# Kernel optimization log

Measured on AMD Instinct MI355X. Metric: run time of the kernel, lower is better.

## Reference

```python
import jax, jax.numpy as jnp
import numpy as np
from jax import lax

NUM_INPUTS = 1024
NUM_OUTPUTS = 1024
NUM_LAYERS = 32          # 1 first + (NUM_LAYERS-1) middle + 1 last, per torch __init__
N = 4096                 # num_neurons_per_layer
W = 65536                # parallel bit-array width


def _nand_layer(x, idx, mask):
    # x: [num_in, W] bool; idx: [num_out, 2] int; mask: [num_out] bool
    g = x[idx]                       # [num_out, 2, W] gather
    out = g[:, 0, :] & g[:, 1, :]    # bitwise AND
    return jnp.where(mask[:, None], ~out, out)  # conditional NOT


def setup_inputs() -> dict:
    key = jax.random.key(0)
    k = jax.random.split(key, 7)
    n_mid = NUM_LAYERS - 1
    return {
        "input_bitarrays": jax.random.bernoulli(k[0], 0.5, (NUM_INPUTS, W)),
        "idx_first": jax.random.randint(k[1], (N, 2), 0, NUM_INPUTS, dtype=jnp.int64 if jax.config.jax_enable_x64 else jnp.int32),
        "mask_first": jax.random.bernoulli(k[2], 0.5, (N,)),
        "idx_mid": jax.random.randint(k[3], (n_mid, N, 2), 0, N, dtype=jnp.int64 if jax.config.jax_enable_x64 else jnp.int32),
        "mask_mid": jax.random.bernoulli(k[4], 0.5, (n_mid, N)),
        "idx_last": jax.random.randint(k[5], (NUM_OUTPUTS, 2), 0, N, dtype=jnp.int64 if jax.config.jax_enable_x64 else jnp.int32),
        "mask_last": jax.random.bernoulli(k[6], 0.5, (NUM_OUTPUTS,)),
    }


def reference(input_bitarrays, idx_first, mask_first, idx_mid, mask_mid, idx_last, mask_last):
    x = _nand_layer(input_bitarrays, idx_first, mask_first)

    def step(carry, params):
        idx, mask = params
        return _nand_layer(carry, idx, mask), None

    x, _ = lax.scan(step, x, (idx_mid, mask_mid))
    return _nand_layer(x, idx_last, mask_last)
```

## Files before the change

### kernel.cpp

```cpp
#include <hip/hip_runtime.h>
#include <stdint.h>

#define NINPUTS   1024
#define NOUTPUTS  1024
#define NMID      31
#define NN        4096
#define W         65536
#define CHUNK     128
#define WPN       4
#define NCHUNKS   (W / CHUNK)
#define GRID      256
#define CPW       (NCHUNKS / GRID)
#define THREADS   1024
#define NPAIRS    16
#define TBL_BYTES ((size_t)NPAIRS * NN * 16)

__global__ void build_tbl_kernel(const int*      __restrict__ idx_first,
                                 const uint32_t* __restrict__ mask_first,
                                 const int*      __restrict__ idx_mid,
                                 const uint32_t* __restrict__ mask_mid,
                                 uint4*          __restrict__ tbl)
{
    const int tid = blockIdx.x * blockDim.x + threadIdx.x;
    const int F = tid >> 12;
    const int n = tid & (NN - 1);

    const int*      i1;
    const uint32_t* m1;
    if (F == 0) { i1 = idx_first; m1 = mask_first; }
    else        { i1 = idx_mid + (size_t)(2 * F - 1) * NN * 2;
                  m1 = mask_mid + (size_t)(2 * F - 1) * NN; }
    const int*      i2 = idx_mid + (size_t)(2 * F) * NN * 2;
    const uint32_t* m2 = mask_mid + (size_t)(2 * F) * NN;

    const int j = i2[2 * n];
    const int k = i2[2 * n + 1];
    uint4 e;
    e.x = (uint32_t)(i1[2 * j]     * 16) | (m1[j] ? 0x80000000u : 0u);
    e.y = (uint32_t)(i1[2 * j + 1] * 16);
    e.z = (uint32_t)(i1[2 * k]     * 16) | (m1[k] ? 0x80000000u : 0u);
    e.w = (uint32_t)(i1[2 * k + 1] * 16) | (m2[n] ? 0x80000000u : 0u);
    tbl[(size_t)F * NN + n] = e;
}

__global__ __launch_bounds__(THREADS, 4)
void nand_fused_kernel(const uint32_t* __restrict__ in,
                       const uint4*    __restrict__ tbl,
                       const int*      __restrict__ idx_last,
                       const uint32_t* __restrict__ mask_last,
                       uint32_t*       __restrict__ out)
{
    __shared__ uint32_t lds[40960];
    uint32_t* P = lds;
    uint32_t* X = lds + 4096;
    uint32_t* Y = lds + 20480;
    uint32_t* R = lds + 36864;

    const int t      = threadIdx.x;
    const int l      = t & 63;
    const int wv     = t >> 6;
    const int lane32 = l & 31;
    const int half   = l >> 5;
    const int shift  = half ? 32 : 0;
    const int bcol   = blockIdx.x * (CPW * CHUNK);

    #pragma unroll 4
    for (int s = 0; s < 32; ++s) {
        const int r = s * 32 + wv * 2 + half;
        const uint4 v = *(const uint4*)(in + (size_t)r * W + bcol + lane32 * 4);
        const unsigned long long b0 = __ballot(v.x != 0u);
        const unsigned long long b1 = __ballot(v.y != 0u);
        const unsigned long long b2 = __ballot(v.z != 0u);
        const unsigned long long b3 = __ballot(v.w != 0u);
        if (lane32 == 0) {
            uint4 w;
            w.x = (uint32_t)(b0 >> shift);
            w.y = (uint32_t)(b1 >> shift);
            w.z = (uint32_t)(b2 >> shift);
            w.w = (uint32_t)(b3 >> shift);
            *(uint4*)&P[r * WPN] = w;
        }
    }
    __syncthreads();

    for (int i = 0; i < CPW; ++i) {
        const int c0n = bcol + (i + 1) * CHUNK;
        const int c0p = bcol + (i - 1) * CHUNK;
        const bool do_pack   = (i + 1 < CPW);
        const bool do_unpack = (i > 0);

        uint4 tc[4], tn[4];
        #pragma unroll
        for (int k = 0; k < 4; ++k) tc[k] = tbl[k * THREADS + t];

        for (int F = 0; F <= 16; ++F) {
            uint4 pv0 = {0,0,0,0}, pv1 = {0,0,0,0};
            int pr0 = 0, pr1 = 0;
            if (do_pack && F >= 1) {
                pr0 = (F - 1) * 64 + wv * 2 + half;
                pr1 = pr0 + 32;
                pv0 = *(const uint4*)(in + (size_t)pr0 * W + c0n + lane32 * 4);
                pv1 = *(const uint4*)(in + (size_t)pr1 * W + c0n + lane32 * 4);
            }

            if (F <= 15) {
                const uint32_t* src = (F == 0) ? P : ((F & 1) ? X : Y);
                uint32_t*       dst = (F & 1) ? Y : X;
                uint4 A[4], B[4], C[4], D[4];
                #pragma unroll
                for (int k = 0; k < 4; ++k) {
                    const uint4 e = tc[k];
                    A[k] = *(const uint4*)((const char*)src + (e.x & 0xFFFFu));
                    B[k] = *(const uint4*)((const char*)src + e.y);
                    C[k] = *(const uint4*)((const char*)src + (e.z & 0xFFFFu));
                    D[k] = *(const uint4*)((const char*)src + (e.w & 0xFFFFu));
                }
                #pragma unroll
                for (int k = 0; k < 4; ++k) {
                    const int n = k * THREADS + t;
                    const uint4 e = tc[k];
                    const uint32_t xm1 = (uint32_t)((int32_t)e.x >> 31);
                    const uint32_t xm2 = (uint32_t)((int32_t)e.z >> 31);
                    const uint32_t xm3 = (uint32_t)((int32_t)e.w >> 31);
                    uint4 r;
                    r.x = (((A[k].x & B[k].x) ^ xm1) & ((C[k].x & D[k].x) ^ xm2)) ^ xm3;
                    r.y = (((A[k].y & B[k].y) ^ xm1) & ((C[k].y & D[k].y) ^ xm2)) ^ xm3;
                    r.z = (((A[k].z & B[k].z) ^ xm1) & ((C[k].z & D[k].z) ^ xm2)) ^ xm3;
                    r.w = (((A[k].w & B[k].w) ^ xm1) & ((C[k].w & D[k].w) ^ xm2)) ^ xm3;
                    *(uint4*)&dst[n * WPN] = r;
                }
            } else {
                const int n = t;
                const int2 ij = ((const int2*)idx_last)[n];
                const uint32_t xm = mask_last[n] ? 0xFFFFFFFFu : 0u;
                const uint4 a = *(const uint4*)&Y[ij.x * WPN];
                const uint4 b = *(const uint4*)&Y[ij.y * WPN];
                uint4 r;
                r.x = (a.x & b.x) ^ xm;  r.y = (a.y & b.y) ^ xm;
                r.z = (a.z & b.z) ^ xm;  r.w = (a.w & b.w) ^ xm;
                *(uint4*)&R[n * WPN] = r;
            }

            if (F <= 14) {
                #pragma unroll
                for (int k = 0; k < 4; ++k)
                    tn[k] = tbl[(size_t)(F + 1) * NN + k * THREADS + t];
            }

            if (do_unpack && F <= 15) {
                #pragma unroll
                for (int s = 0; s < 2; ++s) {
                    const int r = F * 64 + s * 32 + wv * 2 + half;
                    const uint4 w4 = *(const uint4*)&R[r * WPN];
                    uint4 v;
                    v.x = (w4.x >> lane32) & 1u;
                    v.y = (w4.y >> lane32) & 1u;
                    v.z = (w4.z >> lane32) & 1u;
                    v.w = (w4.w >> lane32) & 1u;
                    *(uint4*)(out + (size_t)r * W + c0p + lane32 * 4) = v;
                }
            }

            if (do_pack && F >= 1) {
                {
                    const unsigned long long b0 = __ballot(pv0.x != 0u);
                    const unsigned long long b1 = __ballot(pv0.y != 0u);
                    const unsigned long long b2 = __ballot(pv0.z != 0u);
                    const unsigned long long b3 = __ballot(pv0.w != 0u);
                    if (lane32 == 0) {
                        uint4 w;
                        w.x = (uint32_t)(b0 >> shift);
                        w.y = (uint32_t)(b1 >> shift);
                        w.z = (uint32_t)(b2 >> shift);
                        w.w = (uint32_t)(b3 >> shift);
                        *(uint4*)&P[pr0 * WPN] = w;
                    }
                }
                {
                    const unsigned long long b0 = __ballot(pv1.x != 0u);
                    const unsigned long long b1 = __ballot(pv1.y != 0u);
                    const unsigned long long b2 = __ballot(pv1.z != 0u);
                    const unsigned long long b3 = __ballot(pv1.w != 0u);
                    if (lane32 == 0) {
                        uint4 w;
                        w.x = (uint32_t)(b0 >> shift);
                        w.y = (uint32_t)(b1 >> shift);
                        w.z = (uint32_t)(b2 >> shift);
                        w.w = (uint32_t)(b3 >> shift);
                        *(uint4*)&P[pr1 * WPN] = w;
                    }
                }
            }

            if (F <= 14) {
                #pragma unroll
                for (int k = 0; k < 4; ++k) tc[k] = tn[k];
            }
            __syncthreads();
        }
    }

    {
        const int c0l = bcol + (CPW - 1) * CHUNK;
        #pragma unroll 4
        for (int s = 0; s < 32; ++s) {
            const int r = s * 32 + wv * 2 + half;
            const uint4 w4 = *(const uint4*)&R[r * WPN];
            uint4 v;
            v.x = (w4.x >> lane32) & 1u;
            v.y = (w4.y >> lane32) & 1u;
            v.z = (w4.z >> lane32) & 1u;
            v.w = (w4.w >> lane32) & 1u;
            *(uint4*)(out + (size_t)r * W + c0l + lane32 * 4) = v;
        }
    }
}

__global__ __launch_bounds__(THREADS, 4)
void nand_pipe128_kernel(const uint32_t* __restrict__ in,
                         const int*      __restrict__ idx_first,
                         const uint32_t* __restrict__ mask_first,
                         const int*      __restrict__ idx_mid,
                         const uint32_t* __restrict__ mask_mid,
                         const int*      __restrict__ idx_last,
                         const uint32_t* __restrict__ mask_last,
                         uint32_t*       __restrict__ out)
{
    __shared__ uint32_t lds[40960];
    uint32_t* P = lds;
    uint32_t* X = lds + 4096;
    uint32_t* Y = lds + 20480;
    uint32_t* R = lds + 36864;

    const int t      = threadIdx.x;
    const int l      = t & 63;
    const int wv     = t >> 6;
    const int lane32 = l & 31;
    const int half   = l >> 5;
    const int shift  = half ? 32 : 0;
    const int bcol   = blockIdx.x * (CPW * CHUNK);

    #pragma unroll 4
    for (int s = 0; s < 32; ++s) {
        const int r = s * 32 + wv * 2 + half;
        const uint4 v = *(const uint4*)(in + (size_t)r * W + bcol + lane32 * 4);
        const unsigned long long b0 = __ballot(v.x != 0u);
        const unsigned long long b1 = __ballot(v.y != 0u);
        const unsigned long long b2 = __ballot(v.z != 0u);
        const unsigned long long b3 = __ballot(v.w != 0u);
        if (lane32 == 0) {
            uint4 w;
            w.x = (uint32_t)(b0 >> shift);  w.y = (uint32_t)(b1 >> shift);
            w.z = (uint32_t)(b2 >> shift);  w.w = (uint32_t)(b3 >> shift);
            *(uint4*)&P[r * WPN] = w;
        }
    }
    __syncthreads();

    for (int i = 0; i < CPW; ++i) {
        const int c0n = bcol + (i + 1) * CHUNK;
        const int c0p = bcol + (i - 1) * CHUNK;
        const bool do_pack   = (i + 1 < CPW);
        const bool do_unpack = (i > 0);

        for (int L = 0; L <= 32; ++L) {
            uint4 pv = {0, 0, 0, 0};
            int   pr = 0;
            if (do_pack && L >= 1) {
                pr = (L - 1) * 32 + wv * 2 + half;
                pv = *(const uint4*)(in + (size_t)pr * W + c0n + lane32 * 4);
            }
            if (L == 0) {
                #pragma unroll
                for (int k = 0; k < NN / THREADS; ++k) {
                    const int n = k * THREADS + t;
                    const int2 ij = ((const int2*)idx_first)[n];
                    const uint32_t xm = mask_first[n] ? 0xFFFFFFFFu : 0u;
                    const uint4 a = *(const uint4*)&P[ij.x * WPN];
                    const uint4 b = *(const uint4*)&P[ij.y * WPN];
                    uint4 r;
                    r.x = (a.x & b.x) ^ xm;  r.y = (a.y & b.y) ^ xm;
                    r.z = (a.z & b.z) ^ xm;  r.w = (a.w & b.w) ^ xm;
                    *(uint4*)&X[n * WPN] = r;
                }
            } else if (L <= 31) {
                const int*      idxL = idx_mid + (size_t)(L - 1) * NN * 2;
                const uint32_t* mL   = mask_mid + (size_t)(L - 1) * NN;
                const uint32_t* src  = (L & 1) ? X : Y;
                uint32_t*       dst  = (L & 1) ? Y : X;
                #pragma unroll
                for (int k = 0; k < NN / THREADS; ++k) {
                    const int n = k * THREADS + t;
                    const int2 ij = ((const int2*)idxL)[n];
                    const uint32_t xm = mL[n] ? 0xFFFFFFFFu : 0u;
                    const uint4 a = *(const uint4*)&src[ij.x * WPN];
                    const uint4 b = *(const uint4*)&src[ij.y * WPN];
                    uint4 r;
                    r.x = (a.x & b.x) ^ xm;  r.y = (a.y & b.y) ^ xm;
                    r.z = (a.z & b.z) ^ xm;  r.w = (a.w & b.w) ^ xm;
                    *(uint4*)&dst[n * WPN] = r;
                }
            } else {
                const int n = t;
                const int2 ij = ((const int2*)idx_last)[n];
                const uint32_t xm = mask_last[n] ? 0xFFFFFFFFu : 0u;
                const uint4 a = *(const uint4*)&Y[ij.x * WPN];
                const uint4 b = *(const uint4*)&Y[ij.y * WPN];
                uint4 r;
                r.x = (a.x & b.x) ^ xm;  r.y = (a.y & b.y) ^ xm;
                r.z = (a.z & b.z) ^ xm;  r.w = (a.w & b.w) ^ xm;
                *(uint4*)&R[n * WPN] = r;
            }
            if (do_unpack && L <= 31) {
                const int r = L * 32 + wv * 2 + half;
                const uint4 w4 = *(const uint4*)&R[r * WPN];
                uint4 v;
                v.x = (w4.x >> lane32) & 1u;  v.y = (w4.y >> lane32) & 1u;
                v.z = (w4.z >> lane32) & 1u;  v.w = (w4.w >> lane32) & 1u;
                *(uint4*)(out + (size_t)r * W + c0p + lane32 * 4) = v;
            }
            if (do_pack && L >= 1) {
                const unsigned long long b0 = __ballot(pv.x != 0u);
                const unsigned long long b1 = __ballot(pv.y != 0u);
                const unsigned long long b2 = __ballot(pv.z != 0u);
                const unsigned long long b3 = __ballot(pv.w != 0u);
                if (lane32 == 0) {
                    uint4 w;
                    w.x = (uint32_t)(b0 >> shift);  w.y = (uint32_t)(b1 >> shift);
                    w.z = (uint32_t)(b2 >> shift);  w.w = (uint32_t)(b3 >> shift);
                    *(uint4*)&P[pr * WPN] = w;
                }
            }
            __syncthreads();
        }
    }
    {
        const int c0l = bcol + (CPW - 1) * CHUNK;
        #pragma unroll 4
        for (int s = 0; s < 32; ++s) {
            const int r = s * 32 + wv * 2 + half;
            const uint4 w4 = *(const uint4*)&R[r * WPN];
            uint4 v;
            v.x = (w4.x >> lane32) & 1u;  v.y = (w4.y >> lane32) & 1u;
            v.z = (w4.z >> lane32) & 1u;  v.w = (w4.w >> lane32) & 1u;
            *(uint4*)(out + (size_t)r * W + c0l + lane32 * 4) = v;
        }
    }
}

extern "C" void kernel_launch(void* const* d_in, const int* in_sizes, int n_in,
                              void* d_out, int out_size, void* d_ws, size_t ws_size,
                              hipStream_t stream) {
    const uint32_t* in         = (const uint32_t*)d_in[0];
    const int*      idx_first  = (const int*)d_in[1];
    const uint32_t* mask_first = (const uint32_t*)d_in[2];
    const int*      idx_mid    = (const int*)d_in[3];
    const uint32_t* mask_mid   = (const uint32_t*)d_in[4];
    const int*      idx_last   = (const int*)d_in[5];
    const uint32_t* mask_last  = (const uint32_t*)d_in[6];
    uint32_t*       out        = (uint32_t*)d_out;

    if (ws_size >= TBL_BYTES) {
        uint4* tbl = (uint4*)d_ws;
        build_tbl_kernel<<<(NPAIRS * NN) / 256, 256, 0, stream>>>(
            idx_first, mask_first, idx_mid, mask_mid, tbl);
        nand_fused_kernel<<<GRID, THREADS, 0, stream>>>(
            in, tbl, idx_last, mask_last, out);
    } else {
        nand_pipe128_kernel<<<GRID, THREADS, 0, stream>>>(
            in, idx_first, mask_first, idx_mid, mask_mid, idx_last, mask_last, out);
    }
}
```

Baseline: 151.9 us.

## Store intermediate LDS layers in struct-of-arrays layout with ds_read2st64 gathers

The X and Y intermediate buffers switch from an array-of-structs layout (four words per neuron) to a struct-of-arrays layout where each word plane is strided by 4096 words. Gathers and stores use ds_read2st64/ds_write2st64 inline asm, and the table offsets are rescaled to match. The goal is to cut LDS bank conflicts from random 16-byte gathers. In exchange, each k iteration now waits on lgkmcnt(0) behind a sched_barrier, which limits overlap of LDS loads across the unrolled k loop, and the prefetch of the next table is moved earlier.

```diff
diff --git a/kernel.cpp b/kernel.cpp
--- a/kernel.cpp
+++ b/kernel.cpp
@@ -15,6 +15,9 @@
 #define NPAIRS    16
 #define TBL_BYTES ((size_t)NPAIRS * NN * 16)
 
+#define XB 16384u
+#define YB 81920u
+
 __global__ void build_tbl_kernel(const int*      __restrict__ idx_first,
                                  const uint32_t* __restrict__ mask_first,
                                  const int*      __restrict__ idx_mid,
@@ -33,15 +36,28 @@
     const int*      i2 = idx_mid + (size_t)(2 * F) * NN * 2;
     const uint32_t* m2 = mask_mid + (size_t)(2 * F) * NN;
 
+    const uint32_t scale = (F == 0) ? 16u : 4u;
     const int j = i2[2 * n];
     const int k = i2[2 * n + 1];
     uint4 e;
-    e.x = (uint32_t)(i1[2 * j]     * 16) | (m1[j] ? 0x80000000u : 0u);
-    e.y = (uint32_t)(i1[2 * j + 1] * 16);
-    e.z = (uint32_t)(i1[2 * k]     * 16) | (m1[k] ? 0x80000000u : 0u);
-    e.w = (uint32_t)(i1[2 * k + 1] * 16) | (m2[n] ? 0x80000000u : 0u);
+    e.x = (uint32_t)i1[2 * j]     * scale | (m1[j] ? 0x80000000u : 0u);
+    e.y = (uint32_t)i1[2 * j + 1] * scale;
+    e.z = (uint32_t)i1[2 * k]     * scale | (m1[k] ? 0x80000000u : 0u);
+    e.w = (uint32_t)i1[2 * k + 1] * scale | (m2[n] ? 0x80000000u : 0u);
     tbl[(size_t)F * NN + n] = e;
 }
+
+#define SOA_READ(W01, W23, VA)                                               \
+    asm volatile("ds_read2st64_b32 %0, %1 offset0:0 offset1:64"              \
+                 : "=v"(W01) : "v"(VA));                                     \
+    asm volatile("ds_read2st64_b32 %0, %1 offset0:128 offset1:192"           \
+                 : "=v"(W23) : "v"(VA));
+
+#define SOA_WRITE(DA, R0, R1, R2, R3)                                        \
+    asm volatile("ds_write2st64_b32 %0, %1, %2 offset0:0 offset1:64"         \
+                 :: "v"(DA), "v"(R0), "v"(R1));                              \
+    asm volatile("ds_write2st64_b32 %0, %1, %2 offset0:128 offset1:192"      \
+                 :: "v"(DA), "v"(R2), "v"(R3));
 
 __global__ __launch_bounds__(THREADS, 4)
 void nand_fused_kernel(const uint32_t* __restrict__ in,
@@ -52,8 +68,6 @@
 {
     __shared__ uint32_t lds[40960];
     uint32_t* P = lds;
-    uint32_t* X = lds + 4096;
-    uint32_t* Y = lds + 20480;
     uint32_t* R = lds + 36864;
 
     const int t      = threadIdx.x;
@@ -102,19 +116,13 @@
                 pv0 = *(const uint4*)(in + (size_t)pr0 * W + c0n + lane32 * 4);
                 pv1 = *(const uint4*)(in + (size_t)pr1 * W + c0n + lane32 * 4);
             }
-
-            if (F <= 15) {
-                const uint32_t* src = (F == 0) ? P : ((F & 1) ? X : Y);
-                uint32_t*       dst = (F & 1) ? Y : X;
-                uint4 A[4], B[4], C[4], D[4];
-                #pragma unroll
-                for (int k = 0; k < 4; ++k) {
-                    const uint4 e = tc[k];
-                    A[k] = *(const uint4*)((const char*)src + (e.x & 0xFFFFu));
-                    B[k] = *(const uint4*)((const char*)src + e.y);
-                    C[k] = *(const uint4*)((const char*)src + (e.z & 0xFFFFu));
-                    D[k] = *(const uint4*)((const char*)src + (e.w & 0xFFFFu));
-                }
+            if (F <= 14) {
+                #pragma unroll
+                for (int k = 0; k < 4; ++k)
+                    tn[k] = tbl[(size_t)(F + 1) * NN + k * THREADS + t];
+            }
+
+            if (F == 0) {
                 #pragma unroll
                 for (int k = 0; k < 4; ++k) {
                     const int n = k * THREADS + t;
@@ -122,29 +130,66 @@
                     const uint32_t xm1 = (uint32_t)((int32_t)e.x >> 31);
                     const uint32_t xm2 = (uint32_t)((int32_t)e.z >> 31);
                     const uint32_t xm3 = (uint32_t)((int32_t)e.w >> 31);
-                    uint4 r;
-                    r.x = (((A[k].x & B[k].x) ^ xm1) & ((C[k].x & D[k].x) ^ xm2)) ^ xm3;
-                    r.y = (((A[k].y & B[k].y) ^ xm1) & ((C[k].y & D[k].y) ^ xm2)) ^ xm3;
-                    r.z = (((A[k].z & B[k].z) ^ xm1) & ((C[k].z & D[k].z) ^ xm2)) ^ xm3;
-                    r.w = (((A[k].w & B[k].w) ^ xm1) & ((C[k].w & D[k].w) ^ xm2)) ^ xm3;
-                    *(uint4*)&dst[n * WPN] = r;
+                    const uint4 a = *(const uint4*)((const char*)P + (e.x & 0xFFFFu));
+                    const uint4 b = *(const uint4*)((const char*)P + e.y);
+                    const uint4 c = *(const uint4*)((const char*)P + (e.z & 0xFFFFu));
+                    const uint4 d = *(const uint4*)((const char*)P + (e.w & 0xFFFFu));
+                    const uint32_t r0 = (((a.x & b.x) ^ xm1) & ((c.x & d.x) ^ xm2)) ^ xm3;
+                    const uint32_t r1 = (((a.y & b.y) ^ xm1) & ((c.y & d.y) ^ xm2)) ^ xm3;
+                    const uint32_t r2 = (((a.z & b.z) ^ xm1) & ((c.z & d.z) ^ xm2)) ^ xm3;
+                    const uint32_t r3 = (((a.w & b.w) ^ xm1) & ((c.w & d.w) ^ xm2)) ^ xm3;
+                    const uint32_t da = XB + (uint32_t)n * 4u;
+                    SOA_WRITE(da, r0, r1, r2, r3);
+                }
+            } else if (F <= 15) {
+                const uint32_t sb = (F & 1) ? XB : YB;
+                const uint32_t db = (F & 1) ? YB : XB;
+                #pragma unroll
+                for (int k = 0; k < 4; ++k) {
+                    const int n = k * THREADS + t;
+                    const uint4 e = tc[k];
+                    const uint32_t xm1 = (uint32_t)((int32_t)e.x >> 31);
+                    const uint32_t xm2 = (uint32_t)((int32_t)e.z >> 31);
+                    const uint32_t xm3 = (uint32_t)((int32_t)e.w >> 31);
+                    const uint32_t vaA = sb + (e.x & 0xFFFFu);
+                    const uint32_t vaB = sb + e.y;
+                    const uint32_t vaC = sb + (e.z & 0xFFFFu);
+                    const uint32_t vaD = sb + (e.w & 0xFFFFu);
+                    uint64_t A01, A23, B01, B23, C01, C23, D01, D23;
+                    SOA_READ(A01, A23, vaA);
+                    SOA_READ(B01, B23, vaB);
+                    SOA_READ(C01, C23, vaC);
+                    SOA_READ(D01, D23, vaD);
+                    asm volatile("s_waitcnt lgkmcnt(0)" ::: "memory");
+                    __builtin_amdgcn_sched_barrier(0);
+                    const uint32_t r0 = ((((uint32_t)A01 & (uint32_t)B01) ^ xm1) &
+                                         (((uint32_t)C01 & (uint32_t)D01) ^ xm2)) ^ xm3;
+                    const uint32_t r1 = ((((uint32_t)(A01 >> 32) & (uint32_t)(B01 >> 32)) ^ xm1) &
+                                         (((uint32_t)(C01 >> 32) & (uint32_t)(D01 >> 32)) ^ xm2)) ^ xm3;
+                    const uint32_t r2 = ((((uint32_t)A23 & (uint32_t)B23) ^ xm1) &
+                                         (((uint32_t)C23 & (uint32_t)D23) ^ xm2)) ^ xm3;
+                    const uint32_t r3 = ((((uint32_t)(A23 >> 32) & (uint32_t)(B23 >> 32)) ^ xm1) &
+                                         (((uint32_t)(C23 >> 32) & (uint32_t)(D23 >> 32)) ^ xm2)) ^ xm3;
+                    const uint32_t da = db + (uint32_t)n * 4u;
+                    SOA_WRITE(da, r0, r1, r2, r3);
                 }
             } else {
                 const int n = t;
                 const int2 ij = ((const int2*)idx_last)[n];
                 const uint32_t xm = mask_last[n] ? 0xFFFFFFFFu : 0u;
-                const uint4 a = *(const uint4*)&Y[ij.x * WPN];
-                const uint4 b = *(const uint4*)&Y[ij.y * WPN];
+                const uint32_t vaA = YB + (uint32_t)ij.x * 4u;
+                const uint32_t vaB = YB + (uint32_t)ij.y * 4u;
+                uint64_t A01, A23, B01, B23;
+                SOA_READ(A01, A23, vaA);
+                SOA_READ(B01, B23, vaB);
+                asm volatile("s_waitcnt lgkmcnt(0)" ::: "memory");
+                __builtin_amdgcn_sched_barrier(0);
                 uint4 r;
-                r.x = (a.x & b.x) ^ xm;  r.y = (a.y & b.y) ^ xm;
-                r.z = (a.z & b.z) ^ xm;  r.w = (a.w & b.w) ^ xm;
+                r.x = ((uint32_t)A01        & (uint32_t)B01)        ^ xm;
+                r.y = ((uint32_t)(A01 >> 32) & (uint32_t)(B01 >> 32)) ^ xm;
+                r.z = ((uint32_t)A23        & (uint32_t)B23)        ^ xm;
+                r.w = ((uint32_t)(A23 >> 32) & (uint32_t)(B23 >> 32)) ^ xm;
                 *(uint4*)&R[n * WPN] = r;
-            }
-
-            if (F <= 14) {
-                #pragma unroll
-                for (int k = 0; k < 4; ++k)
-                    tn[k] = tbl[(size_t)(F + 1) * NN + k * THREADS + t];
             }
 
             if (do_unpack && F <= 15) {
```

New measurement: 228.1 us. 50.2% more time.
